# Optimization experiments

Measured on AMD Instinct MI355X. Metric: run time of the kernel, lower is better.

## Reference

```python
import jax, jax.numpy as jnp
import numpy as np

D_MODEL = 1024
N_HEADS = 16
HEAD_DIM = D_MODEL // N_HEADS


def setup_inputs() -> dict:
    key = jax.random.key(0)
    ks = jax.random.split(key, 5)
    x = jax.random.normal(ks[0], (4, 2048, D_MODEL), dtype=jnp.float32)
    # qkv Linear: weight [3*d_model, d_model], bias [3*d_model]
    w_qkv = jax.random.normal(ks[1], (3 * D_MODEL, D_MODEL), dtype=jnp.float32) / np.sqrt(D_MODEL)
    b_qkv = jnp.zeros((3 * D_MODEL,), dtype=jnp.float32)
    w_out = jax.random.normal(ks[2], (D_MODEL, D_MODEL), dtype=jnp.float32) / np.sqrt(D_MODEL)
    b_out = jnp.zeros((D_MODEL,), dtype=jnp.float32)
    return {"x": x, "w_qkv": w_qkv, "b_qkv": b_qkv, "w_out": w_out, "b_out": b_out}


def reference(x, w_qkv, b_qkv, w_out, b_out):
    B, T, C = x.shape
    H, Dh = N_HEADS, HEAD_DIM
    qkv = x @ w_qkv.T + b_qkv                      # [B,T,3C]
    qkv = qkv.reshape(B, T, 3, H, Dh)
    q = jnp.transpose(qkv[:, :, 0], (0, 2, 1, 3))  # [B,H,T,Dh]
    k = jnp.transpose(qkv[:, :, 1], (0, 2, 1, 3))
    v = jnpp_transpose = jnp.transpose(qkv[:, :, 2], (0, 2, 1, 3))
    scale = 1.0 / np.sqrt(Dh).astype(np.float32)
    att = jnp.einsum('bhqd,bhkd->bhqk', q, k) * scale
    causal = jnp.tril(jnp.ones((T, T), dtype=bool))
    att = jnp.where(causal[None, None], att, -jnp.inf)
    att = jax.nn.softmax(att, axis=-1)
    head_out = jnp.einsum('bhqk,bhkd->bhqd', att, v)  # [B,H,T,Dh]
    out = jnp.transpose(head_out, (0, 2, 1, 3)).reshape(B, T, C)
    return out @ w_out.T + b_out
```

## Files before the change

### kernel.cpp

```cpp
#include <hip/hip_runtime.h>
#include <hip/hip_bf16.h>


#define D_MODEL 1024
#define N_HEADS 16
#define HEAD_DIM 64
#define SEQ 2048
#define BATCH 4

typedef __attribute__((ext_vector_type(8))) short bf16x8;
typedef __attribute__((ext_vector_type(4))) float f32x4;
typedef unsigned int uint;

__device__ __forceinline__ short f2bf(float f) {
    union { float f; uint i; } c; c.f = f;
    uint x = c.i;
    x += 0x7fffu + ((x >> 16) & 1u);
    return (short)(x >> 16);
}
__device__ __forceinline__ uint pack2(float a, float b) {
    return (uint)(unsigned short)f2bf(a) | ((uint)(unsigned short)f2bf(b) << 16);
}
__device__ __forceinline__ uint asu(float f) { union { float f; uint i; } c; c.f = f; return c.i; }
__device__ __forceinline__ uint packtr(float lo, float hi) {
    return (asu(lo) >> 16) | (asu(hi) & 0xffff0000u);
}

__device__ __forceinline__ void glds16(const void* g, void* l) {
    __builtin_amdgcn_global_load_lds(
        (const __attribute__((address_space(1))) uint*)g,
        (__attribute__((address_space(3))) uint*)l, 16, 0, 0);
}

__global__ __launch_bounds__(256) void cvt_bf16(const float* __restrict__ src,
                                                short* __restrict__ dst, int n) {
    int i = (blockIdx.x * 256 + threadIdx.x) * 4;
    if (i < n) {
        float4 f = *(const float4*)(src + i);
        uint2 o; o.x = pack2(f.x, f.y); o.y = pack2(f.z, f.w);
        *(uint2*)(dst + i) = o;
    }
}

template <int MODE>
__global__ __launch_bounds__(256, 2) void gemm_bt(
    const short* __restrict__ A, const short* __restrict__ B,
    const float* __restrict__ bias, float* __restrict__ Cp,
    int M, int N, int K,
    short* __restrict__ qp, short* __restrict__ kp, short* __restrict__ vp)
{
    __shared__ short As[128][32];
    __shared__ short Bs[128][32];
    const int tid = threadIdx.x;
    const int wave = tid >> 6, lane = tid & 63;
    const int quad = lane >> 4, l16 = lane & 15;
    const int wm = (wave >> 1) * 64, wn = (wave & 1) * 64;
    const int rowBase = blockIdx.y * 128;
    const int colBase = blockIdx.x * 128;

    const short* gA = A + (size_t)(rowBase + wave * 32 + (lane >> 2)) * K + (lane & 3) * 8;
    const short* gB = B + (size_t)(colBase + wave * 32 + (lane >> 2)) * K + (lane & 3) * 8;
    void* lA0 = &As[wave * 32][0];
    void* lA1 = &As[wave * 32 + 16][0];
    void* lB0 = &Bs[wave * 32][0];
    void* lB1 = &Bs[wave * 32 + 16][0];

    f32x4 acc[4][4] = {};

    for (int k0 = 0; k0 < K; k0 += 32) {
        __syncthreads();
        glds16(gA + k0, lA0);
        glds16(gA + (size_t)16 * K + k0, lA1);
        glds16(gB + k0, lB0);
        glds16(gB + (size_t)16 * K + k0, lB1);
        __syncthreads();
        bf16x8 af[4], bfr[4];
#pragma unroll
        for (int i = 0; i < 4; ++i)
            af[i] = *(const bf16x8*)&As[wm + i * 16 + l16][quad * 8];
#pragma unroll
        for (int j = 0; j < 4; ++j)
            bfr[j] = *(const bf16x8*)&Bs[wn + j * 16 + l16][quad * 8];
#pragma unroll
        for (int i = 0; i < 4; ++i)
#pragma unroll
            for (int j = 0; j < 4; ++j)
                acc[i][j] = __builtin_amdgcn_mfma_f32_16x16x32_bf16(af[i], bfr[j], acc[i][j], 0, 0, 0);
    }

#pragma unroll
    for (int i = 0; i < 4; ++i) {
#pragma unroll
        for (int j = 0; j < 4; ++j) {
#pragma unroll
            for (int r = 0; r < 4; ++r) {
                int row = rowBase + wm + i * 16 + quad * 4 + r;
                int col = colBase + wn + j * 16 + l16;
                float v = acc[i][j][r] + bias[col];
                if (MODE == 0) {
                    Cp[(size_t)row * N + col] = v;
                } else {
                    int which = col >> 10;
                    int h = (col >> 6) & 15;
                    int d = col & 63;
                    int b = row >> 11;
                    int t = row & 2047;
                    short* dst = (which == 0) ? qp : (which == 1) ? kp : vp;
                    dst[((((size_t)b * N_HEADS + h) * SEQ) + t) * HEAD_DIM + d] = f2bf(v);
                }
            }
        }
    }
}

__global__ __launch_bounds__(256, 2) void attn_fwd(
    const short* __restrict__ Q, const short* __restrict__ K,
    const short* __restrict__ V, short* __restrict__ O)
{
    __shared__ short Ks[64][72];
    __shared__ short Vt[64][72];
    __shared__ short Ps[128][72];
    const int tid = threadIdx.x;
    const int wave = tid >> 6, lane = tid & 63;
    const int quad = lane >> 4, l16 = lane & 15;
    const int bh = blockIdx.x;
    const int b = bh >> 4, h = bh & 15;
    const int qt = gridDim.y - 1 - blockIdx.y;
    const int qbase = qt * 128;
    const short* Qh = Q + (size_t)bh * SEQ * HEAD_DIM;
    const short* Kh = K + (size_t)bh * SEQ * HEAD_DIM;
    const short* Vh = V + (size_t)bh * SEQ * HEAD_DIM;

    bf16x8 qf[2][2];
#pragma unroll
    for (int m = 0; m < 2; ++m)
#pragma unroll
        for (int st = 0; st < 2; ++st)
            qf[m][st] = *(const bf16x8*)(Qh + (size_t)(qbase + wave * 32 + m * 16 + l16) * HEAD_DIM + st * 32 + quad * 8);

    f32x4 o[2][4] = {};
    f32x4 lsum4[2] = {};
    const float C1 = 0.125f * 1.44269504f;
    const float C2 = 14.4269504f;

    const int kr = tid >> 2, kc = (tid & 3) * 16;
    const int vk = (tid & 31) * 2, vd = (tid >> 5) * 8;
    const int subw = qbase + wave * 32;

    const int ntiles = 2 * qt + 2;
    int4 kv0 = *(const int4*)(Kh + (size_t)kr * HEAD_DIM + kc);
    int4 kv1 = *(const int4*)(Kh + (size_t)kr * HEAD_DIM + kc + 8);
    int4 vv0 = *(const int4*)(Vh + (size_t)vk * HEAD_DIM + vd);
    int4 vv1 = *(const int4*)(Vh + (size_t)(vk + 1) * HEAD_DIM + vd);

    for (int j = 0; j < ntiles; ++j) {
        const int kb = j * 64;
        __syncthreads();
        *(int4*)&Ks[kr][kc] = kv0;
        *(int4*)&Ks[kr][kc + 8] = kv1;
        {
            const short* va = (const short*)&vv0;
            const short* vb = (const short*)&vv1;
#pragma unroll
            for (int e = 0; e < 8; ++e)
                *(uint*)&Vt[vd + e][vk] =
                    (uint)(unsigned short)va[e] | ((uint)(unsigned short)vb[e] << 16);
        }
        __syncthreads();

        {
            const int kbn = (j + 1 < ntiles) ? kb + 64 : kb;
            kv0 = *(const int4*)(Kh + (size_t)(kbn + kr) * HEAD_DIM + kc);
            kv1 = *(const int4*)(Kh + (size_t)(kbn + kr) * HEAD_DIM + kc + 8);
            vv0 = *(const int4*)(Vh + (size_t)(kbn + vk) * HEAD_DIM + vd);
            vv1 = *(const int4*)(Vh + (size_t)(kbn + vk + 1) * HEAD_DIM + vd);
        }

        if (kb > subw + 31) continue;

        f32x4 s[2][4];
#pragma unroll
        for (int kt = 0; kt < 4; ++kt) {
            bf16x8 kf0 = *(const bf16x8*)&Ks[kt * 16 + l16][quad * 8];
            bf16x8 kf1 = *(const bf16x8*)&Ks[kt * 16 + l16][32 + quad * 8];
#pragma unroll
            for (int m = 0; m < 2; ++m) {
                f32x4 t = {0.f, 0.f, 0.f, 0.f};
                t = __builtin_amdgcn_mfma_f32_16x16x32_bf16(kf0, qf[m][0], t, 0, 0, 0);
                t = __builtin_amdgcn_mfma_f32_16x16x32_bf16(kf1, qf[m][1], t, 0, 0, 0);
                s[m][kt] = t;
            }
        }
#pragma unroll
        for (int m = 0; m < 2; ++m) {
            const int sub = subw + m * 16;
            const int qrow = sub + l16;
            const bool needmask = (kb + 63 > sub);
            const int prow = wave * 32 + m * 16 + l16;
#pragma unroll
            for (int kt = 0; kt < 4; ++kt) {
                float p[4];
#pragma unroll
                for (int r = 0; r < 4; ++r) {
                    float a = __builtin_fmaf(s[m][kt][r], C1, -C2);
                    if (needmask && (kb + kt * 16 + quad * 4 + r > qrow)) a = -1e30f;
                    p[r] = __builtin_exp2f(a);
                    lsum4[m][r] += p[r];
                }
                uint2 u; u.x = packtr(p[0], p[1]); u.y = packtr(p[2], p[3]);
                *(uint2*)&Ps[prow][kt * 16 + quad * 4] = u;
            }
        }
#pragma unroll
        for (int st = 0; st < 2; ++st) {
            bf16x8 pf0 = *(const bf16x8*)&Ps[wave * 32 + l16][st * 32 + quad * 8];
            bf16x8 pf1 = *(const bf16x8*)&Ps[wave * 32 + 16 + l16][st * 32 + quad * 8];
#pragma unroll
            for (int dt = 0; dt < 4; ++dt) {
                bf16x8 vf = *(const bf16x8*)&Vt[dt * 16 + l16][st * 32 + quad * 8];
                o[0][dt] = __builtin_amdgcn_mfma_f32_16x16x32_bf16(pf0, vf, o[0][dt], 0, 0, 0);
                o[1][dt] = __builtin_amdgcn_mfma_f32_16x16x32_bf16(pf1, vf, o[1][dt], 0, 0, 0);
            }
        }
    }

#pragma unroll
    for (int m = 0; m < 2; ++m) {
        float l = lsum4[m][0] + lsum4[m][1] + lsum4[m][2] + lsum4[m][3];
        l += __shfl_xor(l, 16);
        l += __shfl_xor(l, 32);
#pragma unroll
        for (int r = 0; r < 4; ++r) {
            int qloc = quad * 4 + r;
            float lq = __shfl(l, qloc);
            float inv = 1.f / lq;
            int t = qbase + wave * 32 + m * 16 + qloc;
            size_t base = ((size_t)b * SEQ + t) * D_MODEL + h * HEAD_DIM;
#pragma unroll
            for (int dt = 0; dt < 4; ++dt)
                O[base + dt * 16 + l16] = f2bf(o[m][dt][r] * inv);
        }
    }
}

extern "C" void kernel_launch(void* const* d_in, const int* in_sizes, int n_in,
                              void* d_out, int out_size, void* d_ws, size_t ws_size,
                              hipStream_t stream)
{
    const float* x     = (const float*)d_in[0];
    const float* w_qkv = (const float*)d_in[1];
    const float* b_qkv = (const float*)d_in[2];
    const float* w_out = (const float*)d_in[3];
    const float* b_out = (const float*)d_in[4];
    float* out = (float*)d_out;

    const int NX = BATCH * SEQ * D_MODEL;
    const int NWQ = 3 * D_MODEL * D_MODEL;
    const int NWO = D_MODEL * D_MODEL;
    const size_t HE = (size_t)BATCH * N_HEADS * SEQ * HEAD_DIM;

    short* xb    = (short*)d_ws;
    short* wqkvb = xb + NX;
    short* woutb = wqkvb + NWQ;
    short* qp    = woutb + NWO;
    short* kp    = qp + HE;
    short* vp    = kp + HE;
    short* ho    = xb;

    const int M = BATCH * SEQ;

    cvt_bf16<<<NX / 1024, 256, 0, stream>>>(x, xb, NX);
    cvt_bf16<<<NWQ / 1024, 256, 0, stream>>>(w_qkv, wqkvb, NWQ);
    cvt_bf16<<<NWO / 1024, 256, 0, stream>>>(w_out, woutb, NWO);

    gemm_bt<1><<<dim3(3 * D_MODEL / 128, M / 128), 256, 0, stream>>>(
        xb, wqkvb, b_qkv, nullptr, M, 3 * D_MODEL, D_MODEL, qp, kp, vp);

    attn_fwd<<<dim3(BATCH * N_HEADS, SEQ / 128), 256, 0, stream>>>(qp, kp, vp, ho);

    gemm_bt<0><<<dim3(D_MODEL / 128, M / 128), 256, 0, stream>>>(
        ho, woutb, b_out, out, M, D_MODEL, D_MODEL, nullptr, nullptr, nullptr);
}
```

Before: 263.8 us.

## Fuse conversion launches, vectorize GEMM epilogue, compute softmax row sums via MFMA

Merges the three fp32-to-bf16 conversion kernels into a single launch over the contiguous workspace. Swaps the MFMA operand order in the GEMM so each lane holds four consecutive columns, which lets the epilogue use vectorized float4 and uint2 stores. In attention, the per-lane row-sum accumulation is replaced by an extra MFMA against a ones row placed in padded shared memory. This adds extra MFMAs per tile but drops the VALU adds and the shuffle reduction.

```diff
diff --git a/kernel.cpp b/kernel.cpp
--- a/kernel.cpp
+++ b/kernel.cpp
@@ -8,6 +8,10 @@
 #define SEQ 2048
 #define BATCH 4
 
+#define NX (BATCH * SEQ * D_MODEL)
+#define NWQ (3 * D_MODEL * D_MODEL)
+#define NWO (D_MODEL * D_MODEL)
+
 typedef __attribute__((ext_vector_type(8))) short bf16x8;
 typedef __attribute__((ext_vector_type(4))) float f32x4;
 typedef unsigned int uint;
@@ -32,14 +36,18 @@
         (__attribute__((address_space(3))) uint*)l, 16, 0, 0);
 }
 
-__global__ __launch_bounds__(256) void cvt_bf16(const float* __restrict__ src,
-                                                short* __restrict__ dst, int n) {
+__global__ __launch_bounds__(256) void cvt_all(const float* __restrict__ x,
+                                               const float* __restrict__ wq,
+                                               const float* __restrict__ wo,
+                                               short* __restrict__ dst) {
     int i = (blockIdx.x * 256 + threadIdx.x) * 4;
-    if (i < n) {
-        float4 f = *(const float4*)(src + i);
-        uint2 o; o.x = pack2(f.x, f.y); o.y = pack2(f.z, f.w);
-        *(uint2*)(dst + i) = o;
-    }
+    const float* src; int off;
+    if (i < NX)            { src = x;  off = 0; }
+    else if (i < NX + NWQ) { src = wq; off = NX; }
+    else                   { src = wo; off = NX + NWQ; }
+    float4 f = *(const float4*)(src + (i - off));
+    uint2 o; o.x = pack2(f.x, f.y); o.y = pack2(f.z, f.w);
+    *(uint2*)(dst + i) = o;
 }
 
 template <int MODE>
@@ -85,29 +93,32 @@
         for (int i = 0; i < 4; ++i)
 #pragma unroll
             for (int j = 0; j < 4; ++j)
-                acc[i][j] = __builtin_amdgcn_mfma_f32_16x16x32_bf16(af[i], bfr[j], acc[i][j], 0, 0, 0);
+                acc[i][j] = __builtin_amdgcn_mfma_f32_16x16x32_bf16(bfr[j], af[i], acc[i][j], 0, 0, 0);
     }
 
 #pragma unroll
     for (int i = 0; i < 4; ++i) {
 #pragma unroll
         for (int j = 0; j < 4; ++j) {
-#pragma unroll
-            for (int r = 0; r < 4; ++r) {
-                int row = rowBase + wm + i * 16 + quad * 4 + r;
-                int col = colBase + wn + j * 16 + l16;
-                float v = acc[i][j][r] + bias[col];
-                if (MODE == 0) {
-                    Cp[(size_t)row * N + col] = v;
-                } else {
-                    int which = col >> 10;
-                    int h = (col >> 6) & 15;
-                    int d = col & 63;
-                    int b = row >> 11;
-                    int t = row & 2047;
-                    short* dst = (which == 0) ? qp : (which == 1) ? kp : vp;
-                    dst[((((size_t)b * N_HEADS + h) * SEQ) + t) * HEAD_DIM + d] = f2bf(v);
-                }
+            const int row = rowBase + wm + i * 16 + l16;
+            const int col = colBase + wn + j * 16 + quad * 4;
+            float4 bv = *(const float4*)&bias[col];
+            float v0 = acc[i][j][0] + bv.x;
+            float v1 = acc[i][j][1] + bv.y;
+            float v2 = acc[i][j][2] + bv.z;
+            float v3 = acc[i][j][3] + bv.w;
+            if (MODE == 0) {
+                float4 o = {v0, v1, v2, v3};
+                *(float4*)&Cp[(size_t)row * N + col] = o;
+            } else {
+                int which = col >> 10;
+                int h = (col >> 6) & 15;
+                int d = col & 63;
+                int b = row >> 11;
+                int t = row & 2047;
+                short* dst = (which == 0) ? qp : (which == 1) ? kp : vp;
+                uint2 u; u.x = pack2(v0, v1); u.y = pack2(v2, v3);
+                *(uint2*)&dst[((((size_t)b * N_HEADS + h) * SEQ) + t) * HEAD_DIM + d] = u;
             }
         }
     }
@@ -118,7 +129,7 @@
     const short* __restrict__ V, short* __restrict__ O)
 {
     __shared__ short Ks[64][72];
-    __shared__ short Vt[64][72];
+    __shared__ short Vt[80][72];
     __shared__ short Ps[128][72];
     const int tid = threadIdx.x;
     const int wave = tid >> 6, lane = tid & 63;
@@ -131,6 +142,9 @@
     const short* Kh = K + (size_t)bh * SEQ * HEAD_DIM;
     const short* Vh = V + (size_t)bh * SEQ * HEAD_DIM;
 
+    for (int idx = tid; idx < 16 * 72; idx += 256)
+        Vt[64 + idx / 72][idx % 72] = (idx < 72) ? (short)0x3F80 : (short)0;
+
     bf16x8 qf[2][2];
 #pragma unroll
     for (int m = 0; m < 2; ++m)
@@ -139,7 +153,7 @@
             qf[m][st] = *(const bf16x8*)(Qh + (size_t)(qbase + wave * 32 + m * 16 + l16) * HEAD_DIM + st * 32 + quad * 8);
 
     f32x4 o[2][4] = {};
-    f32x4 lsum4[2] = {};
+    f32x4 o4[2] = {};
     const float C1 = 0.125f * 1.44269504f;
     const float C2 = 14.4269504f;
 
@@ -205,7 +219,6 @@
                     float a = __builtin_fmaf(s[m][kt][r], C1, -C2);
                     if (needmask && (kb + kt * 16 + quad * 4 + r > qrow)) a = -1e30f;
                     p[r] = __builtin_exp2f(a);
-                    lsum4[m][r] += p[r];
                 }
                 uint2 u; u.x = packtr(p[0], p[1]); u.y = packtr(p[2], p[3]);
                 *(uint2*)&Ps[prow][kt * 16 + quad * 4] = u;
@@ -215,26 +228,25 @@
         for (int st = 0; st < 2; ++st) {
             bf16x8 pf0 = *(const bf16x8*)&Ps[wave * 32 + l16][st * 32 + quad * 8];
             bf16x8 pf1 = *(const bf16x8*)&Ps[wave * 32 + 16 + l16][st * 32 + quad * 8];
+            bf16x8 vf4 = *(const bf16x8*)&Vt[64 + l16][st * 32 + quad * 8];
 #pragma unroll
             for (int dt = 0; dt < 4; ++dt) {
                 bf16x8 vf = *(const bf16x8*)&Vt[dt * 16 + l16][st * 32 + quad * 8];
                 o[0][dt] = __builtin_amdgcn_mfma_f32_16x16x32_bf16(pf0, vf, o[0][dt], 0, 0, 0);
                 o[1][dt] = __builtin_amdgcn_mfma_f32_16x16x32_bf16(pf1, vf, o[1][dt], 0, 0, 0);
             }
+            o4[0] = __builtin_amdgcn_mfma_f32_16x16x32_bf16(pf0, vf4, o4[0], 0, 0, 0);
+            o4[1] = __builtin_amdgcn_mfma_f32_16x16x32_bf16(pf1, vf4, o4[1], 0, 0, 0);
         }
     }
 
 #pragma unroll
     for (int m = 0; m < 2; ++m) {
-        float l = lsum4[m][0] + lsum4[m][1] + lsum4[m][2] + lsum4[m][3];
-        l += __shfl_xor(l, 16);
-        l += __shfl_xor(l, 32);
 #pragma unroll
         for (int r = 0; r < 4; ++r) {
-            int qloc = quad * 4 + r;
-            float lq = __shfl(l, qloc);
+            float lq = __shfl(o4[m][r], quad << 4);
             float inv = 1.f / lq;
-            int t = qbase + wave * 32 + m * 16 + qloc;
+            int t = qbase + wave * 32 + m * 16 + quad * 4 + r;
             size_t base = ((size_t)b * SEQ + t) * D_MODEL + h * HEAD_DIM;
 #pragma unroll
             for (int dt = 0; dt < 4; ++dt)
@@ -254,9 +266,6 @@
     const float* b_out = (const float*)d_in[4];
     float* out = (float*)d_out;
 
-    const int NX = BATCH * SEQ * D_MODEL;
-    const int NWQ = 3 * D_MODEL * D_MODEL;
-    const int NWO = D_MODEL * D_MODEL;
     const size_t HE = (size_t)BATCH * N_HEADS * SEQ * HEAD_DIM;
 
     short* xb    = (short*)d_ws;
@@ -269,9 +278,7 @@
 
     const int M = BATCH * SEQ;
 
-    cvt_bf16<<<NX / 1024, 256, 0, stream>>>(x, xb, NX);
-    cvt_bf16<<<NWQ / 1024, 256, 0, stream>>>(w_qkv, wqkvb, NWQ);
-    cvt_bf16<<<NWO / 1024, 256, 0, stream>>>(w_out, woutb, NWO);
+    cvt_all<<<(NX + NWQ + NWO) / 1024, 256, 0, stream>>>(x, w_qkv, w_out, xb);
 
     gemm_bt<1><<<dim3(3 * D_MODEL / 128, M / 128), 256, 0, stream>>>(
         xb, wqkvb, b_qkv, nullptr, M, 3 * D_MODEL, D_MODEL, qp, kp, vp);
```

Result: no change. 264.2 us (+0.2%).
